# Kernel optimization log

Measured on AMD Instinct MI355X. Metric: run time of the kernel, lower is better.

## Reference

```python
import jax, jax.numpy as jnp
import numpy as np

VOCAB = 32000
EMB = 1024
BLOCK = 2048
B = 4


def setup_inputs() -> dict:
    key = jax.random.key(0)
    ks = jax.random.split(key, 10)
    s = EMB ** -0.5
    return {
        "idx": jax.random.randint(ks[0], (B, BLOCK), 0, VOCAB),
        "targets": jax.random.randint(ks[1], (B, BLOCK), 0, VOCAB),
        "tok_emb": jax.random.normal(ks[2], (VOCAB, EMB), jnp.float32),
        "pos_emb": jax.random.normal(ks[3], (BLOCK, EMB), jnp.float32),
        "Wk": jax.random.normal(ks[4], (EMB, EMB), jnp.float32) * s,
        "Wq": jax.random.normal(ks[5], (EMB, EMB), jnp.float32) * s,
        "Wv": jax.random.normal(ks[6], (EMB, EMB), jnp.float32) * s,
        "Wlm": jax.random.normal(ks[7], (EMB, VOCAB), jnp.float32) * s,
        "blm": jnp.zeros((VOCAB,), jnp.float32),
    }


def reference(idx, targets, tok_emb, pos_emb, Wk, Wq, Wv, Wlm, blm):
    B_, T = idx.shape
    x = tok_emb[idx] + pos_emb[:T]  # [B,T,C]
    C = x.shape[-1]
    k = x @ Wk  # [B,T,H]
    q = x @ Wq
    v = x @ Wv
    wei = jnp.einsum("bth,bsh->bts", q, k) * (C ** -0.5)  # [B,T,T]
    causal = jnp.tril(jnp.ones((T, T), bool))
    wei = jnp.where(causal, wei, -jnp.inf)
    wei = jax.nn.softmax(wei, axis=-1)
    out = jnp.einsum("bts,bsh->bth", wei, v)  # [B,T,H]
    logits = out @ Wlm + blm  # [B,T,V]
    logits2d = logits.reshape(B_ * T, -1)
    tgt = targets.reshape(B_ * T)
    logp = jax.nn.log_softmax(logits2d, axis=-1)
    loss = -jnp.mean(jnp.take_along_axis(logp, tgt[:, None], axis=1))
    return logits2d, loss
```

## Files before the change

kernel.cpp:

```cpp
#include <hip/hip_runtime.h>
#include <hip/hip_bf16.h>
#include <cstdint>

#define VOCAB 32000
#define EMB   1024
#define TLEN  2048
#define NB    4
#define MTOT  (NB*TLEN)

typedef __bf16 bf16;
typedef __bf16 bf16x8 __attribute__((ext_vector_type(8)));
typedef float  f32x4  __attribute__((ext_vector_type(4)));

__global__ void embed_kernel(const int* __restrict__ idx,
                             const float* __restrict__ tok,
                             const float* __restrict__ pos,
                             bf16* __restrict__ x)
{
    int gid = blockIdx.x * 256 + threadIdx.x;
    int r   = gid >> 7;
    int c0  = (gid & 127) << 3;
    int t   = r & (TLEN - 1);
    int tk  = idx[r];
    const float4* tp = reinterpret_cast<const float4*>(tok + (long)tk * EMB + c0);
    const float4* pp = reinterpret_cast<const float4*>(pos + (long)t  * EMB + c0);
    float4 a0 = tp[0], a1 = tp[1];
    float4 b0 = pp[0], b1 = pp[1];
    bf16x8 o;
    o[0] = (bf16)(a0.x + b0.x); o[1] = (bf16)(a0.y + b0.y);
    o[2] = (bf16)(a0.z + b0.z); o[3] = (bf16)(a0.w + b0.w);
    o[4] = (bf16)(a1.x + b1.x); o[5] = (bf16)(a1.y + b1.y);
    o[6] = (bf16)(a1.z + b1.z); o[7] = (bf16)(a1.w + b1.w);
    *reinterpret_cast<bf16x8*>(x + (long)r * EMB + c0) = o;
}

__global__ void transpose_conv_kernel(const float* __restrict__ W,
                                      bf16* __restrict__ Wt,
                                      int Kdim, int Ndim)
{
    __shared__ bf16 tile[64][65];
    int n0 = blockIdx.x * 64;
    int k0 = blockIdx.y * 64;
    int tid = threadIdx.x;
    int c  = tid & 63, r0 = tid >> 6;
#pragma unroll
    for (int i = 0; i < 16; ++i) {
        int r = r0 + i * 4;
        tile[r][c] = (bf16)W[(long)(k0 + r) * Ndim + n0 + c];
    }
    __syncthreads();
    int kc = tid & 63, nr0 = tid >> 6;
#pragma unroll
    for (int i = 0; i < 16; ++i) {
        int nr = nr0 + i * 4;
        Wt[(long)(n0 + nr) * Kdim + k0 + kc] = tile[kc][nr];
    }
}

__device__ __forceinline__ void gll16(const void* g, void* l)
{
    __builtin_amdgcn_global_load_lds(
        (const __attribute__((address_space(1))) unsigned int*)g,
        (__attribute__((address_space(3))) unsigned int*)l, 16, 0, 0);
}

template<int OMODE>
__global__ __launch_bounds__(256)
void gemm_bt_kernel(const bf16* __restrict__ A, int lda, long sA,
                    const bf16* __restrict__ Bt, int ldb, long sB,
                    void* __restrict__ Cv, int ldc, long sC,
                    int K, const float* __restrict__ bias)
{
    __shared__ bf16 As[128 * 32];
    __shared__ bf16 Bs[128 * 32];

    const int tid  = threadIdx.x;
    const int lane = tid & 63;
    const int wv   = tid >> 6;
    const int wr   = wv >> 1, wc = wv & 1;
    const long zb  = blockIdx.z;

    const bf16* Ab = A  + zb * sA + (long)(blockIdx.y * 128) * lda;
    const bf16* Bb = Bt + zb * sB + (long)(blockIdx.x * 128) * ldb;

    f32x4 acc[4][4] = {};

    const int l0 = tid, l1 = tid + 256;
    const int r0s = l0 >> 2, kg0 = (l0 & 3) * 8;
    const int r1s = l1 >> 2, kg1 = (l1 & 3) * 8;

    for (int kt = 0; kt < K; kt += 32) {
        if (kt) __syncthreads();
        gll16(Ab + (long)r0s * lda + kt + kg0, &As[l0 * 8]);
        gll16(Ab + (long)r1s * lda + kt + kg1, &As[l1 * 8]);
        gll16(Bb + (long)r0s * ldb + kt + kg0, &Bs[l0 * 8]);
        gll16(Bb + (long)r1s * ldb + kt + kg1, &Bs[l1 * 8]);
        __syncthreads();

        bf16x8 af[4], bfr[4];
#pragma unroll
        for (int i = 0; i < 4; ++i) {
            af[i]  = *reinterpret_cast<const bf16x8*>(
                         &As[(wr * 64 + i * 16 + (lane & 15)) * 32 + (lane >> 4) * 8]);
            bfr[i] = *reinterpret_cast<const bf16x8*>(
                         &Bs[(wc * 64 + i * 16 + (lane & 15)) * 32 + (lane >> 4) * 8]);
        }
#pragma unroll
        for (int i = 0; i < 4; ++i)
#pragma unroll
            for (int j = 0; j < 4; ++j)
                acc[i][j] = __builtin_amdgcn_mfma_f32_16x16x32_bf16(
                                af[i], bfr[j], acc[i][j], 0, 0, 0);
    }

    const int rowb = blockIdx.y * 128 + wr * 64 + ((lane >> 4) << 2);
    const int colb = blockIdx.x * 128 + wc * 64 + (lane & 15);

    if (OMODE == 0) {
        bf16* C = (bf16*)Cv + zb * sC;
#pragma unroll
        for (int i = 0; i < 4; ++i)
#pragma unroll
            for (int j = 0; j < 4; ++j)
#pragma unroll
                for (int r = 0; r < 4; ++r)
                    C[(long)(rowb + i * 16 + r) * ldc + colb + j * 16] = (bf16)acc[i][j][r];
    } else {
        float* C = (float*)Cv + zb * sC;
#pragma unroll
        for (int i = 0; i < 4; ++i)
#pragma unroll
            for (int j = 0; j < 4; ++j)
#pragma unroll
                for (int r = 0; r < 4; ++r)
                    C[(long)(rowb + i * 16 + r) * ldc + colb + j * 16] = acc[i][j][r];
    }
}

__device__ __forceinline__ void stage_kh(const bf16* __restrict__ g, int koff,
                                         bf16* l, int tid)
{
#pragma unroll
    for (int p = 0; p < 2; ++p) {
        int lin = p * 512 + tid;
        int row = lin >> 2, gr = lin & 3;
        gll16(g + (long)row * EMB + koff + gr * 8, l + lin * 8);
    }
}

__global__ __launch_bounds__(512)
void gemm256_logits(const bf16* __restrict__ A, const bf16* __restrict__ Bt,
                    float* __restrict__ C, const float* __restrict__ bias,
                    float2* __restrict__ part)
{
    extern __shared__ bf16 smem[];
    bf16* As = smem;
    bf16* Bs = smem + 32768;

    const int tid  = threadIdx.x;
    const int lane = tid & 63, wid = tid >> 6;
    const int wr = wid >> 2, wc = wid & 3;
    const int l15 = lane & 15, hi = lane >> 4;

    const int wg = blockIdx.x;
    const int xcd = wg & 7, c = wg >> 3;
    const int nb = c >> 2;
    const int mb = xcd * 4 + (c & 3);

    const bf16* Ab = A  + (long)(mb * 256) * EMB;
    const bf16* Bb = Bt + (long)(nb * 256) * EMB;

    f32x4 acc[8][4] = {};
    bf16x8 af[4], bfr[4];

    const int aoff = (wr * 128 + l15) * 32 + hi * 8;
    const int boff = (wc * 64  + l15) * 32 + hi * 8;

#define DSA(b,kh,m)  (*(const bf16x8*)(As + (b)*16384 + (kh)*8192 + (m)*512 + aoff))
#define DSB(b,kh,n)  (*(const bf16x8*)(Bs + (b)*16384 + (kh)*8192 + (n)*512 + boff))

#define MFMA_Q(mbase)                                                        \
    __builtin_amdgcn_s_setprio(1);                                           \
    _Pragma("unroll")                                                        \
    for (int m_ = 0; m_ < 4; ++m_)                                           \
        _Pragma("unroll")                                                    \
        for (int n_ = 0; n_ < 4; ++n_)                                       \
            acc[(mbase) + m_][n_] = __builtin_amdgcn_mfma_f32_16x16x32_bf16( \
                af[m_], bfr[n_], acc[(mbase) + m_][n_], 0, 0, 0);            \
    __builtin_amdgcn_s_setprio(0);

#define PHASE_BAR                                                            \
    __builtin_amdgcn_s_barrier();                                            \
    asm volatile("s_waitcnt lgkmcnt(0)" ::: "memory");                       \
    __builtin_amdgcn_sched_barrier(0);

#define TILE(b, kt, DOSTAGE, LAST)                                           \
    {                                                                        \
                                                          \
        _Pragma("unroll") for (int n_=0;n_<4;++n_) bfr[n_] = DSB(b,0,n_);    \
        _Pragma("unroll") for (int m_=0;m_<4;++m_) af[m_]  = DSA(b,0,m_);    \
        if (DOSTAGE) stage_kh(Ab, (kt)+64, As + ((b)^1)*16384, tid);         \
        PHASE_BAR; MFMA_Q(0);                                                \
        __builtin_amdgcn_s_barrier();                                        \
                                              \
        if (LAST) { asm volatile("s_waitcnt vmcnt(0)" ::: "memory"); }       \
        else      { asm volatile("s_waitcnt vmcnt(2)" ::: "memory"); }       \
        _Pragma("unroll") for (int m_=0;m_<4;++m_) af[m_]  = DSA(b,0,4+m_);  \
        if (DOSTAGE) stage_kh(Bb, (kt)+64, Bs + ((b)^1)*16384, tid);         \
        PHASE_BAR; MFMA_Q(4);                                                \
        __builtin_amdgcn_s_barrier();                                        \
                                                          \
        _Pragma("unroll") for (int n_=0;n_<4;++n_) bfr[n_] = DSB(b,1,n_);    \
        _Pragma("unroll") for (int m_=0;m_<4;++m_) af[m_]  = DSA(b,1,m_);    \
        if (DOSTAGE) stage_kh(Ab, (kt)+96, As + ((b)^1)*16384 + 8192, tid);  \
        PHASE_BAR; MFMA_Q(0);                                                \
        __builtin_amdgcn_s_barrier();                                        \
                                                          \
        if (!LAST) { asm volatile("s_waitcnt vmcnt(2)" ::: "memory"); }      \
        _Pragma("unroll") for (int m_=0;m_<4;++m_) af[m_]  = DSA(b,1,4+m_);  \
        if (DOSTAGE) stage_kh(Bb, (kt)+96, Bs + ((b)^1)*16384 + 8192, tid);  \
        PHASE_BAR; MFMA_Q(4);                                                \
        __builtin_amdgcn_s_barrier();                                        \
    }

    stage_kh(Ab, 0,  As, tid);
    stage_kh(Bb, 0,  Bs, tid);
    stage_kh(Ab, 32, As + 8192, tid);
    stage_kh(Bb, 32, Bs + 8192, tid);
    asm volatile("s_waitcnt vmcnt(4)" ::: "memory");
    __builtin_amdgcn_s_barrier();

#pragma unroll 1
    for (int it = 0; it < 7; ++it) {
        const int kt = it * 128;
        TILE(0, kt, 1, 0);
        TILE(1, kt + 64, 1, 0);
    }
    TILE(0, 896, 1, 0);
    TILE(1, 960, 0, 1);

#undef TILE
#undef PHASE_BAR
#undef MFMA_Q
#undef DSA
#undef DSB

    float* pm = (float*)smem;
    float* ps = pm + 1024;

    const long colbase = (long)nb * 256 + wc * 64 + l15;
    float bv[4];
#pragma unroll
    for (int n = 0; n < 4; ++n) bv[n] = bias[colbase + n * 16];

    const long rowbase = (long)mb * 256 + wr * 128;
#pragma unroll
    for (int m = 0; m < 8; ++m) {
#pragma unroll
        for (int r = 0; r < 4; ++r) {
            float v0 = acc[m][0][r] + bv[0];
            float v1 = acc[m][1][r] + bv[1];
            float v2 = acc[m][2][r] + bv[2];
            float v3 = acc[m][3][r] + bv[3];
            long row = rowbase + m * 16 + (hi << 2) + r;
            float* Cp = C + row * (long)VOCAB + colbase;
            Cp[0] = v0; Cp[16] = v1; Cp[32] = v2; Cp[48] = v3;

            float lm = fmaxf(fmaxf(v0, v1), fmaxf(v2, v3));
#pragma unroll
            for (int o = 1; o < 16; o <<= 1) lm = fmaxf(lm, __shfl_xor(lm, o));
            float sp = __expf(v0 - lm) + __expf(v1 - lm) +
                       __expf(v2 - lm) + __expf(v3 - lm);
#pragma unroll
            for (int o = 1; o < 16; o <<= 1) sp += __shfl_xor(sp, o);
            if (l15 == 0) {
                int rb = wr * 128 + m * 16 + (hi << 2) + r;
                pm[wc * 256 + rb] = lm;
                ps[wc * 256 + rb] = sp;
            }
        }
    }
    __syncthreads();
    if (tid < 256) {
        float m0 = pm[tid], m1 = pm[256 + tid], m2 = pm[512 + tid], m3 = pm[768 + tid];
        float M = fmaxf(fmaxf(m0, m1), fmaxf(m2, m3));
        float S = ps[tid] * __expf(m0 - M) + ps[256 + tid] * __expf(m1 - M) +
                  ps[512 + tid] * __expf(m2 - M) + ps[768 + tid] * __expf(m3 - M);
        part[((long)mb * 256 + tid) * 125 + nb] = make_float2(M, S);
    }
}

__global__ void softmax_causal_kernel(const bf16* __restrict__ S,
                                      bf16* __restrict__ P)
{
    const int r = blockIdx.x;
    const int t = r & (TLEN - 1);
    const int tid = threadIdx.x;
    const int lane = tid & 63, wv = tid >> 6;
    const float scale = 0.03125f;
    const int c0 = tid * 8;
    bf16x8 sv = *(const bf16x8*)(S + (long)r * TLEN + c0);

    float v[8];
    float m = -1e30f;
#pragma unroll
    for (int i = 0; i < 8; ++i) {
        float x = (c0 + i <= t) ? (float)sv[i] * scale : -1e30f;
        v[i] = x;
        m = fmaxf(m, x);
    }
    __shared__ float red[4];
#pragma unroll
    for (int off = 32; off; off >>= 1) m = fmaxf(m, __shfl_xor(m, off));
    if (lane == 0) red[wv] = m;
    __syncthreads();
    m = fmaxf(fmaxf(red[0], red[1]), fmaxf(red[2], red[3]));
    __syncthreads();

    float s = 0.f;
#pragma unroll
    for (int i = 0; i < 8; ++i) { v[i] = __expf(v[i] - m); s += v[i]; }
#pragma unroll
    for (int off = 32; off; off >>= 1) s += __shfl_xor(s, off);
    if (lane == 0) red[wv] = s;
    __syncthreads();
    s = red[0] + red[1] + red[2] + red[3];
    float inv = 1.0f / s;
    bf16x8 o;
#pragma unroll
    for (int i = 0; i < 8; ++i) o[i] = (bf16)(v[i] * inv);
    *(bf16x8*)(P + (long)r * TLEN + c0) = o;
}

__global__ void loss_combine_kernel(const float2* __restrict__ part,
                                    const float* __restrict__ logits,
                                    const int* __restrict__ tgt,
                                    float* __restrict__ bsum)
{
    const int tid = threadIdx.x;
    const int row = blockIdx.x * 256 + tid;
    const int lane = tid & 63, wv = tid >> 6;
    const float2* p = part + (long)row * 125;
    float M = -1e30f, S = 0.f;
    for (int i = 0; i < 125; ++i) {
        float2 v = p[i];
        if (v.x <= M) S += v.y * __expf(v.x - M);
        else { S = S * __expf(M - v.x) + v.y; M = v.x; }
    }
    float lse = M + __logf(S);
    float l = lse - logits[(long)row * VOCAB + tgt[row]];
#pragma unroll
    for (int off = 32; off; off >>= 1) l += __shfl_xor(l, off);
    __shared__ float red[4];
    if (lane == 0) red[wv] = l;
    __syncthreads();
    if (tid == 0) bsum[blockIdx.x] = red[0] + red[1] + red[2] + red[3];
}

__global__ void loss_final_kernel(const float* __restrict__ bsum,
                                  float* __restrict__ out)
{
    const int lane = threadIdx.x;
    float s = (lane < 32) ? bsum[lane] : 0.f;
#pragma unroll
    for (int off = 32; off; off >>= 1) s += __shfl_xor(s, off);
    if (lane == 0) out[0] = s * (1.0f / MTOT);
}

extern "C" void kernel_launch(void* const* d_in, const int* in_sizes, int n_in,
                              void* d_out, int out_size, void* d_ws, size_t ws_size,
                              hipStream_t stream)
{
    const int*   idx = (const int*)  d_in[0];
    const int*   tgt = (const int*)  d_in[1];
    const float* tok = (const float*)d_in[2];
    const float* pos = (const float*)d_in[3];
    const float* Wk  = (const float*)d_in[4];
    const float* Wq  = (const float*)d_in[5];
    const float* Wv  = (const float*)d_in[6];
    const float* Wlm = (const float*)d_in[7];
    const float* blm = (const float*)d_in[8];
    float* out = (float*)d_out;

    char* ws = (char*)d_ws;
    if (ws_size < (size_t)140 * 1024 * 1024) return;

    bf16*   x     = (bf16*)(ws);
    bf16*   qk    = (bf16*)(ws + (16l << 20));
    bf16*   v_t   = (bf16*)(ws + (48l << 20));
    bf16*   S     = (bf16*)(ws + (64l << 20));
    bf16*   Wqk_t = (bf16*)(ws + (96l << 20));
    bf16*   Wv_t  = (bf16*)(ws + (100l << 20));
    bf16*   att   = (bf16*)(ws);
    bf16*   P     = (bf16*)(ws + (16l << 20));
    bf16*   Wlm_t = (bf16*)(ws + (48l << 20));
    float2* part  = (float2*)(ws + (112l << 20));
    float*  bsum  = (float*)(ws + (120l << 20));

    embed_kernel<<<dim3(MTOT * EMB / 8 / 256), 256, 0, stream>>>(idx, tok, pos, x);

    transpose_conv_kernel<<<dim3(16, 16), 256, 0, stream>>>(Wq, Wqk_t, EMB, EMB);
    transpose_conv_kernel<<<dim3(16, 16), 256, 0, stream>>>(Wk, Wqk_t + 1024 * 1024, EMB, EMB);
    transpose_conv_kernel<<<dim3(16, 16), 256, 0, stream>>>(Wv, Wv_t, EMB, EMB);

    gemm_bt_kernel<0><<<dim3(2048 / 128, MTOT / 128, 1), 256, 0, stream>>>(
        x, EMB, 0, Wqk_t, EMB, 0, qk, 2048, 0, EMB, nullptr);
    gemm_bt_kernel<0><<<dim3(MTOT / 128, EMB / 128, 1), 256, 0, stream>>>(
        Wv_t, EMB, 0, x, EMB, 0, v_t, MTOT, 0, EMB, nullptr);

    gemm_bt_kernel<0><<<dim3(TLEN / 128, TLEN / 128, NB), 256, 0, stream>>>(
        qk, 2048, (long)TLEN * 2048, qk + 1024, 2048, (long)TLEN * 2048,
        S, TLEN, (long)TLEN * TLEN, EMB, nullptr);

    softmax_causal_kernel<<<dim3(MTOT), 256, 0, stream>>>(S, P);

    gemm_bt_kernel<0><<<dim3(EMB / 128, TLEN / 128, NB), 256, 0, stream>>>(
        P, TLEN, (long)TLEN * TLEN, v_t, MTOT, (long)TLEN,
        att, EMB, (long)TLEN * EMB, TLEN, nullptr);

    transpose_conv_kernel<<<dim3(VOCAB / 64, EMB / 64), 256, 0, stream>>>(
        Wlm, Wlm_t, EMB, VOCAB);

    gemm256_logits<<<dim3(4000), 512, 131072, stream>>>(att, Wlm_t, out, blm, part);

    loss_combine_kernel<<<dim3(32), 256, 0, stream>>>(part, out, tgt, bsum);
    loss_final_kernel<<<dim3(1), 64, 0, stream>>>(bsum, out + (long)MTOT * VOCAB);
}
```

Before: 1.012 ms.

## Use XOR-swizzled 64-wide K tiles in logits GEMM shared memory staging

Replaces the two 32-wide K half-tile staging with a single 64-wide K tile per buffer, stored with an XOR swizzle of 16-byte slots by row so LDS fragment reads avoid bank conflicts. The stage loads are now issued in two of the four phases and drained with a full vmcnt(0) wait at tile end, instead of fine-grained vmcnt(2) waits. This aims to cut LDS bank conflicts and simplify the pipeline, at the cost of less overlap between global loads and compute. The loop also uses runtime buffer parity (it&1) inside an unroll-1 loop.

```diff
diff --git a/kernel.cpp b/kernel.cpp
--- a/kernel.cpp
+++ b/kernel.cpp
@@ -137,14 +137,16 @@
     }
 }
 
-__device__ __forceinline__ void stage_kh(const bf16* __restrict__ g, int koff,
-                                         bf16* l, int tid)
-{
-#pragma unroll
-    for (int p = 0; p < 2; ++p) {
-        int lin = p * 512 + tid;
-        int row = lin >> 2, gr = lin & 3;
-        gll16(g + (long)row * EMB + koff + gr * 8, l + lin * 8);
+__device__ __forceinline__ void stage256(const bf16* __restrict__ gbase, int kt,
+                                         bf16* lbase, int tid)
+{
+#pragma unroll
+    for (int p = 0; p < 4; ++p) {
+        int lin  = p * 512 + tid;
+        int row  = lin >> 3;
+        int slot = lin & 7;
+        int ke   = ((slot ^ (row & 7)) << 3) + kt;
+        gll16(gbase + (long)row * EMB + ke, lbase + lin * 8);
     }
 }
 
@@ -160,7 +162,7 @@
     const int tid  = threadIdx.x;
     const int lane = tid & 63, wid = tid >> 6;
     const int wr = wid >> 2, wc = wid & 3;
-    const int l15 = lane & 15, hi = lane >> 4;
+    const int l15 = lane & 15, hi = lane >> 4, l7 = lane & 7;
 
     const int wg = blockIdx.x;
     const int xcd = wg & 7, c = wg >> 3;
@@ -173,11 +175,10 @@
     f32x4 acc[8][4] = {};
     bf16x8 af[4], bfr[4];
 
-    const int aoff = (wr * 128 + l15) * 32 + hi * 8;
-    const int boff = (wc * 64  + l15) * 32 + hi * 8;
-
-#define DSA(b,kh,m)  (*(const bf16x8*)(As + (b)*16384 + (kh)*8192 + (m)*512 + aoff))
-#define DSB(b,kh,n)  (*(const bf16x8*)(Bs + (b)*16384 + (kh)*8192 + (n)*512 + boff))
+    const int ko0 = 8 * (hi ^ l7);
+    const int ko1 = 8 * ((4 | hi) ^ l7);
+    const bf16* Ap = As + (wr * 128 + l15) * 64;
+    const bf16* Bp = Bs + (wc * 64  + l15) * 64;
 
 #define MFMA_Q(mbase)                                                        \
     __builtin_amdgcn_s_setprio(1);                                           \
@@ -194,56 +195,51 @@
     asm volatile("s_waitcnt lgkmcnt(0)" ::: "memory");                       \
     __builtin_amdgcn_sched_barrier(0);
 
-#define TILE(b, kt, DOSTAGE, LAST)                                           \
+#define TILE(b, kt, DOSTAGE)                                                 \
     {                                                                        \
-                                                          \
-        _Pragma("unroll") for (int n_=0;n_<4;++n_) bfr[n_] = DSB(b,0,n_);    \
-        _Pragma("unroll") for (int m_=0;m_<4;++m_) af[m_]  = DSA(b,0,m_);    \
-        if (DOSTAGE) stage_kh(Ab, (kt)+64, As + ((b)^1)*16384, tid);         \
+                              \
+        _Pragma("unroll") for (int n_=0;n_<4;++n_)                           \
+            bfr[n_] = *(const bf16x8*)(Bp + (b)*16384 + n_*1024 + ko0);      \
+        _Pragma("unroll") for (int m_=0;m_<4;++m_)                           \
+            af[m_]  = *(const bf16x8*)(Ap + (b)*16384 + m_*1024 + ko0);      \
+        if (DOSTAGE) stage256(Ab, (kt)+64, As + ((b)^1)*16384, tid);         \
         PHASE_BAR; MFMA_Q(0);                                                \
         __builtin_amdgcn_s_barrier();                                        \
-                                              \
-        if (LAST) { asm volatile("s_waitcnt vmcnt(0)" ::: "memory"); }       \
-        else      { asm volatile("s_waitcnt vmcnt(2)" ::: "memory"); }       \
-        _Pragma("unroll") for (int m_=0;m_<4;++m_) af[m_]  = DSA(b,0,4+m_);  \
-        if (DOSTAGE) stage_kh(Bb, (kt)+64, Bs + ((b)^1)*16384, tid);         \
+                          \
+        _Pragma("unroll") for (int m_=0;m_<4;++m_)                           \
+            af[m_]  = *(const bf16x8*)(Ap + (b)*16384 + (4+m_)*1024 + ko0);  \
+        if (DOSTAGE) stage256(Bb, (kt)+64, Bs + ((b)^1)*16384, tid);         \
         PHASE_BAR; MFMA_Q(4);                                                \
         __builtin_amdgcn_s_barrier();                                        \
-                                                          \
-        _Pragma("unroll") for (int n_=0;n_<4;++n_) bfr[n_] = DSB(b,1,n_);    \
-        _Pragma("unroll") for (int m_=0;m_<4;++m_) af[m_]  = DSA(b,1,m_);    \
-        if (DOSTAGE) stage_kh(Ab, (kt)+96, As + ((b)^1)*16384 + 8192, tid);  \
+                                                  \
+        _Pragma("unroll") for (int n_=0;n_<4;++n_)                           \
+            bfr[n_] = *(const bf16x8*)(Bp + (b)*16384 + n_*1024 + ko1);      \
+        _Pragma("unroll") for (int m_=0;m_<4;++m_)                           \
+            af[m_]  = *(const bf16x8*)(Ap + (b)*16384 + m_*1024 + ko1);      \
         PHASE_BAR; MFMA_Q(0);                                                \
         __builtin_amdgcn_s_barrier();                                        \
-                                                          \
-        if (!LAST) { asm volatile("s_waitcnt vmcnt(2)" ::: "memory"); }      \
-        _Pragma("unroll") for (int m_=0;m_<4;++m_) af[m_]  = DSA(b,1,4+m_);  \
-        if (DOSTAGE) stage_kh(Bb, (kt)+96, Bs + ((b)^1)*16384 + 8192, tid);  \
+               \
+        _Pragma("unroll") for (int m_=0;m_<4;++m_)                           \
+            af[m_]  = *(const bf16x8*)(Ap + (b)*16384 + (4+m_)*1024 + ko1);  \
         PHASE_BAR; MFMA_Q(4);                                                \
+        if (DOSTAGE) { asm volatile("s_waitcnt vmcnt(0)" ::: "memory"); }    \
         __builtin_amdgcn_s_barrier();                                        \
     }
 
-    stage_kh(Ab, 0,  As, tid);
-    stage_kh(Bb, 0,  Bs, tid);
-    stage_kh(Ab, 32, As + 8192, tid);
-    stage_kh(Bb, 32, Bs + 8192, tid);
-    asm volatile("s_waitcnt vmcnt(4)" ::: "memory");
+    stage256(Ab, 0, As, tid);
+    stage256(Bb, 0, Bs, tid);
+    asm volatile("s_waitcnt vmcnt(0)" ::: "memory");
     __builtin_amdgcn_s_barrier();
 
 #pragma unroll 1
-    for (int it = 0; it < 7; ++it) {
-        const int kt = it * 128;
-        TILE(0, kt, 1, 0);
-        TILE(1, kt + 64, 1, 0);
-    }
-    TILE(0, 896, 1, 0);
-    TILE(1, 960, 0, 1);
+    for (int it = 0; it < 15; ++it) {
+        TILE((it & 1), it * 64, 1);
+    }
+    TILE(1, 960, 0);
 
 #undef TILE
 #undef PHASE_BAR
 #undef MFMA_Q
-#undef DSA
-#undef DSB
 
     float* pm = (float*)smem;
     float* ps = pm + 1024;
```

Result: faster. 971.4 us (-4.0%).
